# Kernel optimization log

Measured on AMD Instinct MI355X. Metric: run time of the kernel, lower is better.

## Reference

```python
import jax, jax.numpy as jnp
from jax import lax
import numpy as np
import math

# Static module config (matches init_kwargs)
K = 5            # kernel_size
MD = 3           # max_degree
HH = (MD + 1) ** 2   # n_harmonics = 16
CIN, F = 16, 32
B, D = 1, 48
NJ = K // 2      # n_radial_profiles (one shell per integer radius 1..K//2)
DN = ('NCDHW', 'OIDHW', 'NCDHW')


def _sh_table(ct, st, phi):
    """Complex spherical harmonics Y_n^m up to degree 3 (Condon-Shortley), [*grid, HH]."""
    fourpi = 4.0 * np.pi
    def N(n, m):
        return np.sqrt((2 * n + 1) / fourpi * math.factorial(n - m) / math.factorial(n + m))
    P = {
        (0, 0): np.ones_like(ct),
        (1, 0): ct,
        (1, 1): -st,
        (2, 0): 0.5 * (3 * ct ** 2 - 1),
        (2, 1): -3.0 * ct * st,
        (2, 2): 3.0 * st ** 2,
        (3, 0): 0.5 * (5 * ct ** 3 - 3 * ct),
        (3, 1): -1.5 * (5 * ct ** 2 - 1) * st,
        (3, 2): 15.0 * ct * st ** 2,
        (3, 3): -15.0 * st ** 3,
    }
    sh = np.zeros(ct.shape + (HH,), dtype=np.complex64)
    for n in range(MD + 1):
        for m in range(0, n + 1):
            y = (N(n, m) * P[(n, m)]).astype(np.complex64) * np.exp(1j * m * phi).astype(np.complex64)
            sh[..., n * n + n + m] = y
            if m > 0:
                sh[..., n * n + n - m] = ((-1) ** m) * np.conj(y)
    return sh


def _make_atoms():
    """Radial-shell x SH atoms: [K,K,K,NJ,HH] complex, L2-normalized per atom."""
    g = np.linspace(-(K // 2), K // 2, K)
    x, y, z = np.meshgrid(g, g, g, indexing='xy')
    r = np.sqrt(x * x + y * y + z * z)
    phi = np.arctan2(y, x)
    ct = np.divide(z, r, out=np.zeros_like(r), where=r != 0)
    st = np.sqrt(np.clip(1.0 - ct * ct, 0.0, None))
    sh = _sh_table(ct, st, phi)                                     # [K,K,K,HH]
    prof = np.stack([np.clip(1.0 - np.abs(r - j), 0.0, None) for j in range(1, NJ + 1)], -1)  # [K,K,K,NJ]
    atoms = prof[..., :, None] * sh[..., None, :]                   # [K,K,K,NJ,HH]
    norm = np.sqrt((np.abs(atoms) ** 2).sum(axis=(0, 1, 2), keepdims=True))
    atoms = atoms / np.where(norm > 0, norm, 1.0)
    return atoms.real.astype(np.float32), atoms.imag.astype(np.float32)


ATOMS_R, ATOMS_I = _make_atoms()
DEG = np.repeat(np.arange(MD + 1), 2 * np.arange(MD + 1) + 1)       # harmonic index -> degree (len HH)


def setup_inputs() -> dict:
    key = jax.random.key(0)
    ks = jax.random.split(key, 4)
    lim = float(np.sqrt(6.0 / (CIN + F)))
    return {
        'x': jax.random.normal(ks[0], (B, CIN, D, D, D), jnp.float32),
        'w': jax.random.uniform(ks[1], (CIN, F, NJ, MD + 1), jnp.float32, -lim, lim),
        'central_w': jax.random.uniform(ks[2], (F, CIN, 1, 1, 1), jnp.float32, -lim, lim),
        'central_b': jnp.zeros((F,), jnp.float32),
        'spec_bias': jnp.zeros(((MD + 1) * F,), jnp.float32),
        'proj_w': jax.random.uniform(ks[3], (F, (MD + 1) * F, 1, 1, 1), jnp.float32, -0.1, 0.1),
        'proj_b': jnp.zeros((F,), jnp.float32),
    }


def _forward(x, w, central_w, central_b, spec_bias, proj_w, proj_b):
    # Expand per-degree weights to per-harmonic (repeat_interleave over 2n+1 orders),
    # then fuse the per-channel SH conv + channel/radial weighted sum into a single
    # dense conv with composed kernels (same math as the torch loop + sum over axes 4,6).
    wh = w[..., DEG]                                                 # [C,F,NJ,HH]
    kr = jnp.einsum('cfjh,xyzjh->fhcxyz', wh, jnp.asarray(ATOMS_R)).reshape(F * HH, CIN, K, K, K)
    ki = jnp.einsum('cfjh,xyzjh->fhcxyz', wh, jnp.asarray(ATOMS_I)).reshape(F * HH, CIN, K, K, K)
    yr = lax.conv_general_dilated(x, kr, (1, 1, 1), 'SAME', dimension_numbers=DN)
    yi = lax.conv_general_dilated(x, ki, (1, 1, 1), 'SAME', dimension_numbers=DN)
    b, _, d, h, wd = yr.shape
    yr = yr.reshape(b, F, HH, d, h, wd)
    yi = yi.reshape(b, F, HH, d, h, wd)
    # 1x1x1 central-pixel conv added to the degree-0 (harmonic 0) real map
    cp = lax.conv_general_dilated(x, central_w, (1, 1, 1), 'SAME', dimension_numbers=DN)
    cp = cp + central_b[None, :, None, None, None]
    yr = yr.at[:, :, 0].add(cp)
    # rotation-invariant power spectrum per degree: 1/(2n+1) * sum_m (re^2 + im^2)
    p = yr * yr + yi * yi                                            # [B,F,HH,d,h,w]
    spec = jnp.stack([p[:, :, n * n:n * n + 2 * n + 1].sum(2) / (2 * n + 1) for n in range(MD + 1)], 2)
    spec = spec.reshape(b, F * (MD + 1), d, h, wd) + spec_bias[None, :, None, None, None]
    # activation=('Linear',...) is identity; projection 1x1x1 conv + ReLU
    out = lax.conv_general_dilated(spec, proj_w, (1, 1, 1), 'SAME', dimension_numbers=DN)
    out = out + proj_b[None, :, None, None, None]
    return jax.nn.relu(out)


def reference(x, w, central_w, central_b, spec_bias, proj_w, proj_b):
    return _forward(x, w, central_w, central_b, spec_bias, proj_w, proj_b)
```

## Files before the change

kernel.cpp:

```cpp
#include <hip/hip_runtime.h>
#include <hip/hip_fp16.h>
#include <math.h>


#define TX 8
#define TY 4
#define TZ 4
#define LXX 12
#define LYY 8
#define LZZ 8
#define NPOS 768
#define CPAD 24
#define POSB 48

#define ATAB2_B 0
#define WT2_B   23552
#define CW2_B   31744
#define PWT_B   32768
#define OB_B    49152
#define ED_B    49280

typedef __half2 h2;
union I4H { int4 v; h2 h[4]; };

__global__ __launch_bounds__(256) void ssh_init(
    const float* __restrict__ w, const float* __restrict__ cw,
    const float* __restrict__ proj_w, const float* __restrict__ spec_bias,
    const float* __restrict__ proj_b, char* __restrict__ wsb)
{
    __shared__ float shr[125][16];
    __shared__ float shi[125][16];
    __shared__ float prof[125][2];
    __shared__ float norms[2][16];
    __shared__ int epos[92];
    const int tid = threadIdx.x;
    const float fourpi = 4.0f * 3.14159265358979323846f;

    for (int p = tid; p < 125; p += 256) {
        int d2 = p % 5, d1 = (p / 5) % 5, d0 = p / 25;
        float xc = (float)(d1 - 2), yc = (float)(d0 - 2), zc = (float)(d2 - 2);
        float r2 = xc*xc + yc*yc + zc*zc;
        float r  = sqrtf(r2);
        float phi = atan2f(yc, xc);
        float ct = (r > 0.f) ? (zc / r) : 0.f;
        float st = sqrtf(fmaxf(0.f, 1.f - ct*ct));
        float c1 = cosf(phi), s1 = sinf(phi);
        float c2 = c1*c1 - s1*s1, s2 = 2.f*s1*c1;
        float c3 = c2*c1 - s2*s1, s3 = s2*c1 + c2*s1;
        float P10 = ct,              P11 = -st;
        float P20 = 0.5f*(3.f*ct*ct - 1.f), P21 = -3.f*ct*st, P22 = 3.f*st*st;
        float P30 = 0.5f*(5.f*ct*ct*ct - 3.f*ct);
        float P31 = -1.5f*(5.f*ct*ct - 1.f)*st;
        float P32 = 15.f*ct*st*st;
        float P33 = -15.f*st*st*st;
        float N00 = sqrtf(1.f/fourpi);
        float N10 = sqrtf(3.f/fourpi);
        float N11 = sqrtf(3.f/fourpi * 0.5f);
        float N20 = sqrtf(5.f/fourpi);
        float N21 = sqrtf(5.f/fourpi / 6.f);
        float N22 = sqrtf(5.f/fourpi / 24.f);
        float N30 = sqrtf(7.f/fourpi);
        float N31 = sqrtf(7.f/fourpi / 12.f);
        float N32 = sqrtf(7.f/fourpi / 120.f);
        float N33 = sqrtf(7.f/fourpi / 720.f);
        float b;
        shr[p][0] = N00;               shi[p][0] = 0.f;
        shr[p][2] = N10*P10;           shi[p][2] = 0.f;
        b = N11*P11;
        shr[p][3] =  b*c1;             shi[p][3] =  b*s1;
        shr[p][1] = -b*c1;             shi[p][1] =  b*s1;
        shr[p][6] = N20*P20;           shi[p][6] = 0.f;
        b = N21*P21;
        shr[p][7] =  b*c1;             shi[p][7] =  b*s1;
        shr[p][5] = -b*c1;             shi[p][5] =  b*s1;
        b = N22*P22;
        shr[p][8] =  b*c2;             shi[p][8] =  b*s2;
        shr[p][4] =  b*c2;             shi[p][4] = -b*s2;
        shr[p][12] = N30*P30;          shi[p][12] = 0.f;
        b = N31*P31;
        shr[p][13] =  b*c1;            shi[p][13] =  b*s1;
        shr[p][11] = -b*c1;            shi[p][11] =  b*s1;
        b = N32*P32;
        shr[p][14] =  b*c2;            shi[p][14] =  b*s2;
        shr[p][10] =  b*c2;            shi[p][10] = -b*s2;
        b = N33*P33;
        shr[p][15] =  b*c3;            shi[p][15] =  b*s3;
        shr[p][9]  = -b*c3;            shi[p][9]  =  b*s3;
        prof[p][0] = fmaxf(0.f, 1.f - fabsf(r - 1.f));
        prof[p][1] = fmaxf(0.f, 1.f - fabsf(r - 2.f));
    }
    __syncthreads();

    if (tid < 32) {
        int j = tid >> 4, h = tid & 15;
        float acc = 0.f;
        for (int p = 0; p < 125; ++p) {
            float pr = prof[p][j];
            acc += pr*pr*(shr[p][h]*shr[p][h] + shi[p][h]*shi[p][h]);
        }
        float nn = sqrtf(acc);
        norms[j][h] = (nn > 0.f) ? nn : 1.f;
    }
    if (tid < 125) {
        int p = tid;
        int d2 = p % 5, d1 = (p / 5) % 5, d0 = p / 25;
        int ix = d1 - 2, iy = d0 - 2, iz = d2 - 2;
        int r2i = ix*ix + iy*iy + iz*iz;
        int cls = (r2i == 1) ? 0 : (r2i == 2 || r2i == 3) ? 1
                : (r2i == 4 || r2i == 5 || r2i == 6 || r2i == 8) ? 2 : -1;
        if (cls >= 0) {
            int rank = (cls == 0) ? 0 : (cls == 1) ? 6 : 26;
            for (int q = 0; q < p; ++q) {
                int e2 = q % 5, e1 = (q / 5) % 5, e0 = q / 25;
                int jx = e1 - 2, jy = e0 - 2, jz = e2 - 2;
                int s2i = jx*jx + jy*jy + jz*jz;
                int c2i = (s2i == 1) ? 0 : (s2i == 2 || s2i == 3) ? 1
                       : (s2i == 4 || s2i == 5 || s2i == 6 || s2i == 8) ? 2 : -1;
                rank += (c2i == cls) ? 1 : 0;
            }
            epos[rank] = p;
            ((int*)(wsb + ED_B))[rank] = (d0*(LYY*LXX) + d1*LXX + d2) * POSB;
        }
    }
    __syncthreads();

    h2* at2 = (h2*)(wsb + ATAB2_B);
    for (int t = tid; t < 92*16; t += 256) {
        int e = t >> 4, h = t & 15;
        int p = epos[e];
        float c0 = prof[p][0] / norms[0][h];
        float c1v = prof[p][1] / norms[1][h];
        at2[(h*92+e)*4 + 0] = __float2half2_rn(c0*shr[p][h]);
        at2[(h*92+e)*4 + 1] = __float2half2_rn(c0*shi[p][h]);
        at2[(h*92+e)*4 + 2] = __float2half2_rn(c1v*shr[p][h]);
        at2[(h*92+e)*4 + 3] = __float2half2_rn(c1v*shi[p][h]);
    }
    h2* wt2h = (h2*)(wsb + WT2_B);
    for (int t = tid; t < 2048; t += 256) {
        int n = t >> 9, f = (t >> 4) & 31, j = (t >> 3) & 1, cp = t & 7;
        float a = w[((2*cp*32 + f)*2 + j)*4 + n];
        float b = w[(((2*cp+1)*32 + f)*2 + j)*4 + n];
        wt2h[t] = __halves2half2(__float2half(a), __float2half(b));
    }
    h2* cw2h = (h2*)(wsb + CW2_B);
    for (int t = tid; t < 256; t += 256) {
        int f = t >> 3, cp = t & 7;
        cw2h[t] = __halves2half2(__float2half(cw[f*16 + 2*cp]),
                                 __float2half(cw[f*16 + 2*cp + 1]));
    }
    float* pwT = (float*)(wsb + PWT_B);
    for (int t = tid; t < 4096; t += 256) {
        int i = t >> 5, fo = t & 31;
        pwT[t] = proj_w[fo*128 + i];
    }
    if (tid < 32) {
        float acc = proj_b[tid];
        for (int i = 0; i < 128; ++i) acc += proj_w[tid*128 + i] * spec_bias[i];
        ((float*)(wsb + OB_B))[tid] = acc;
    }
}


__device__ __forceinline__ void conv2c(const __half* __restrict__ ldsh, int baseb,
    const int4* __restrict__ aA, const int4* __restrict__ aB,
    const int* __restrict__ ed, h2 (&zA)[4][8], h2 (&zB)[4][8])
{
#pragma unroll
    for (int r = 0; r < 4; ++r)
#pragma unroll
        for (int q = 0; q < 8; ++q) { zA[r][q] = __float2half2_rn(0.f); zB[r][q] = __float2half2_rn(0.f); }

#pragma unroll 3
    for (int e = 0; e < 6; ++e) {
        I4H ca, cb_, x0, x1;
        ca.v = aA[e]; cb_.v = aB[e];
        const int4* p = (const int4*)((const char*)ldsh + baseb + ed[e]);
        x0.v = p[0]; x1.v = p[1];
#pragma unroll
        for (int q = 0; q < 4; ++q) {
            zA[0][q]   = __hfma2(ca.h[0],  x0.h[q], zA[0][q]);
            zA[1][q]   = __hfma2(ca.h[1],  x0.h[q], zA[1][q]);
            zB[0][q]   = __hfma2(cb_.h[0], x0.h[q], zB[0][q]);
            zB[1][q]   = __hfma2(cb_.h[1], x0.h[q], zB[1][q]);
            zA[0][q+4] = __hfma2(ca.h[0],  x1.h[q], zA[0][q+4]);
            zA[1][q+4] = __hfma2(ca.h[1],  x1.h[q], zA[1][q+4]);
            zB[0][q+4] = __hfma2(cb_.h[0], x1.h[q], zB[0][q+4]);
            zB[1][q+4] = __hfma2(cb_.h[1], x1.h[q], zB[1][q+4]);
        }
    }
#pragma unroll 4
    for (int e = 6; e < 26; ++e) {
        I4H ca, cb_, x0, x1;
        ca.v = aA[e]; cb_.v = aB[e];
        const int4* p = (const int4*)((const char*)ldsh + baseb + ed[e]);
        x0.v = p[0]; x1.v = p[1];
#pragma unroll
        for (int q = 0; q < 4; ++q) {
            zA[0][q]   = __hfma2(ca.h[0],  x0.h[q], zA[0][q]);
            zA[1][q]   = __hfma2(ca.h[1],  x0.h[q], zA[1][q]);
            zA[2][q]   = __hfma2(ca.h[2],  x0.h[q], zA[2][q]);
            zA[3][q]   = __hfma2(ca.h[3],  x0.h[q], zA[3][q]);
            zB[0][q]   = __hfma2(cb_.h[0], x0.h[q], zB[0][q]);
            zB[1][q]   = __hfma2(cb_.h[1], x0.h[q], zB[1][q]);
            zB[2][q]   = __hfma2(cb_.h[2], x0.h[q], zB[2][q]);
            zB[3][q]   = __hfma2(cb_.h[3], x0.h[q], zB[3][q]);
            zA[0][q+4] = __hfma2(ca.h[0],  x1.h[q], zA[0][q+4]);
            zA[1][q+4] = __hfma2(ca.h[1],  x1.h[q], zA[1][q+4]);
            zA[2][q+4] = __hfma2(ca.h[2],  x1.h[q], zA[2][q+4]);
            zA[3][q+4] = __hfma2(ca.h[3],  x1.h[q], zA[3][q+4]);
            zB[0][q+4] = __hfma2(cb_.h[0], x1.h[q], zB[0][q+4]);
            zB[1][q+4] = __hfma2(cb_.h[1], x1.h[q], zB[1][q+4]);
            zB[2][q+4] = __hfma2(cb_.h[2], x1.h[q], zB[2][q+4]);
            zB[3][q+4] = __hfma2(cb_.h[3], x1.h[q], zB[3][q+4]);
        }
    }
#pragma unroll 3
    for (int e = 26; e < 92; ++e) {
        I4H ca, cb_, x0, x1;
        ca.v = aA[e]; cb_.v = aB[e];
        const int4* p = (const int4*)((const char*)ldsh + baseb + ed[e]);
        x0.v = p[0]; x1.v = p[1];
#pragma unroll
        for (int q = 0; q < 4; ++q) {
            zA[2][q]   = __hfma2(ca.h[2],  x0.h[q], zA[2][q]);
            zA[3][q]   = __hfma2(ca.h[3],  x0.h[q], zA[3][q]);
            zB[2][q]   = __hfma2(cb_.h[2], x0.h[q], zB[2][q]);
            zB[3][q]   = __hfma2(cb_.h[3], x0.h[q], zB[3][q]);
            zA[2][q+4] = __hfma2(ca.h[2],  x1.h[q], zA[2][q+4]);
            zA[3][q+4] = __hfma2(ca.h[3],  x1.h[q], zA[3][q+4]);
            zB[2][q+4] = __hfma2(cb_.h[2], x1.h[q], zB[2][q+4]);
            zB[3][q+4] = __hfma2(cb_.h[3], x1.h[q], zB[3][q+4]);
        }
    }
}

__device__ __forceinline__ void conv1c(const __half* __restrict__ ldsh, int baseb,
    const int4* __restrict__ aA, const int* __restrict__ ed, h2 (&zA)[4][8])
{
#pragma unroll
    for (int r = 0; r < 4; ++r)
#pragma unroll
        for (int q = 0; q < 8; ++q) zA[r][q] = __float2half2_rn(0.f);

#pragma unroll 3
    for (int e = 0; e < 6; ++e) {
        I4H ca, x0, x1;
        ca.v = aA[e];
        const int4* p = (const int4*)((const char*)ldsh + baseb + ed[e]);
        x0.v = p[0]; x1.v = p[1];
#pragma unroll
        for (int q = 0; q < 4; ++q) {
            zA[0][q]   = __hfma2(ca.h[0], x0.h[q], zA[0][q]);
            zA[1][q]   = __hfma2(ca.h[1], x0.h[q], zA[1][q]);
            zA[0][q+4] = __hfma2(ca.h[0], x1.h[q], zA[0][q+4]);
            zA[1][q+4] = __hfma2(ca.h[1], x1.h[q], zA[1][q+4]);
        }
    }
#pragma unroll 4
    for (int e = 6; e < 26; ++e) {
        I4H ca, x0, x1;
        ca.v = aA[e];
        const int4* p = (const int4*)((const char*)ldsh + baseb + ed[e]);
        x0.v = p[0]; x1.v = p[1];
#pragma unroll
        for (int q = 0; q < 4; ++q) {
            zA[0][q]   = __hfma2(ca.h[0], x0.h[q], zA[0][q]);
            zA[1][q]   = __hfma2(ca.h[1], x0.h[q], zA[1][q]);
            zA[2][q]   = __hfma2(ca.h[2], x0.h[q], zA[2][q]);
            zA[3][q]   = __hfma2(ca.h[3], x0.h[q], zA[3][q]);
            zA[0][q+4] = __hfma2(ca.h[0], x1.h[q], zA[0][q+4]);
            zA[1][q+4] = __hfma2(ca.h[1], x1.h[q], zA[1][q+4]);
            zA[2][q+4] = __hfma2(ca.h[2], x1.h[q], zA[2][q+4]);
            zA[3][q+4] = __hfma2(ca.h[3], x1.h[q], zA[3][q+4]);
        }
    }
#pragma unroll 3
    for (int e = 26; e < 92; ++e) {
        I4H ca, x0, x1;
        ca.v = aA[e];
        const int4* p = (const int4*)((const char*)ldsh + baseb + ed[e]);
        x0.v = p[0]; x1.v = p[1];
#pragma unroll
        for (int q = 0; q < 4; ++q) {
            zA[2][q]   = __hfma2(ca.h[2], x0.h[q], zA[2][q]);
            zA[3][q]   = __hfma2(ca.h[3], x0.h[q], zA[3][q]);
            zA[2][q+4] = __hfma2(ca.h[2], x1.h[q], zA[2][q+4]);
            zA[3][q+4] = __hfma2(ca.h[3], x1.h[q], zA[3][q+4]);
        }
    }
}

__device__ __forceinline__ void conv2r(const __half* __restrict__ ldsh, int baseb,
    const int4* __restrict__ aA, const int4* __restrict__ aB,
    const int* __restrict__ ed, h2 (&z)[4][8])
{
#pragma unroll
    for (int r = 0; r < 4; ++r)
#pragma unroll
        for (int q = 0; q < 8; ++q) z[r][q] = __float2half2_rn(0.f);

#pragma unroll 3
    for (int e = 0; e < 6; ++e) {
        I4H ca, cb_, x0, x1;
        ca.v = aA[e]; cb_.v = aB[e];
        const int4* p = (const int4*)((const char*)ldsh + baseb + ed[e]);
        x0.v = p[0]; x1.v = p[1];
#pragma unroll
        for (int q = 0; q < 4; ++q) {
            z[0][q]   = __hfma2(ca.h[0],  x0.h[q], z[0][q]);
            z[2][q]   = __hfma2(cb_.h[0], x0.h[q], z[2][q]);
            z[0][q+4] = __hfma2(ca.h[0],  x1.h[q], z[0][q+4]);
            z[2][q+4] = __hfma2(cb_.h[0], x1.h[q], z[2][q+4]);
        }
    }
#pragma unroll 4
    for (int e = 6; e < 26; ++e) {
        I4H ca, cb_, x0, x1;
        ca.v = aA[e]; cb_.v = aB[e];
        const int4* p = (const int4*)((const char*)ldsh + baseb + ed[e]);
        x0.v = p[0]; x1.v = p[1];
#pragma unroll
        for (int q = 0; q < 4; ++q) {
            z[0][q]   = __hfma2(ca.h[0],  x0.h[q], z[0][q]);
            z[1][q]   = __hfma2(ca.h[2],  x0.h[q], z[1][q]);
            z[2][q]   = __hfma2(cb_.h[0], x0.h[q], z[2][q]);
            z[3][q]   = __hfma2(cb_.h[2], x0.h[q], z[3][q]);
            z[0][q+4] = __hfma2(ca.h[0],  x1.h[q], z[0][q+4]);
            z[1][q+4] = __hfma2(ca.h[2],  x1.h[q], z[1][q+4]);
            z[2][q+4] = __hfma2(cb_.h[0], x1.h[q], z[2][q+4]);
            z[3][q+4] = __hfma2(cb_.h[2], x1.h[q], z[3][q+4]);
        }
    }
#pragma unroll 3
    for (int e = 26; e < 92; ++e) {
        I4H ca, cb_, x0, x1;
        ca.v = aA[e]; cb_.v = aB[e];
        const int4* p = (const int4*)((const char*)ldsh + baseb + ed[e]);
        x0.v = p[0]; x1.v = p[1];
#pragma unroll
        for (int q = 0; q < 4; ++q) {
            z[1][q]   = __hfma2(ca.h[2],  x0.h[q], z[1][q]);
            z[3][q]   = __hfma2(cb_.h[2], x0.h[q], z[3][q]);
            z[1][q+4] = __hfma2(ca.h[2],  x1.h[q], z[1][q+4]);
            z[3][q+4] = __hfma2(cb_.h[2], x1.h[q], z[3][q+4]);
        }
    }
}


#define CDEL (2*(LYY*LXX) + 2*LXX + 2)

template<int N>
__device__ __forceinline__ void mixc2(const h2 (&zA)[4][8], const h2 (&zB)[4][8],
    const int4* __restrict__ wt2n, const float* __restrict__ pwT, float2 (&outa)[16])
{
    const float W = 2.f / (float)(2*N + 1);
#pragma unroll 2
    for (int f = 0; f < 32; ++f) {
        I4H w00, w01, w10, w11;
        w00.v = wt2n[f*4+0]; w01.v = wt2n[f*4+1];
        w10.v = wt2n[f*4+2]; w11.v = wt2n[f*4+3];
        h2 yrA = __float2half2_rn(0.f), yiA = __float2half2_rn(0.f);
        h2 yrB = __float2half2_rn(0.f), yiB = __float2half2_rn(0.f);
#pragma unroll
        for (int q = 0; q < 4; ++q) {
            yrA = __hfma2(w00.h[q], zA[0][q],   yrA);
            yrA = __hfma2(w01.h[q], zA[0][q+4], yrA);
            yrA = __hfma2(w10.h[q], zA[2][q],   yrA);
            yrA = __hfma2(w11.h[q], zA[2][q+4], yrA);
            yiA = __hfma2(w00.h[q], zA[1][q],   yiA);
            yiA = __hfma2(w01.h[q], zA[1][q+4], yiA);
            yiA = __hfma2(w10.h[q], zA[3][q],   yiA);
            yiA = __hfma2(w11.h[q], zA[3][q+4], yiA);
            yrB = __hfma2(w00.h[q], zB[0][q],   yrB);
            yrB = __hfma2(w01.h[q], zB[0][q+4], yrB);
            yrB = __hfma2(w10.h[q], zB[2][q],   yrB);
            yrB = __hfma2(w11.h[q], zB[2][q+4], yrB);
            yiB = __hfma2(w00.h[q], zB[1][q],   yiB);
            yiB = __hfma2(w01.h[q], zB[1][q+4], yiB);
            yiB = __hfma2(w10.h[q], zB[3][q],   yiB);
            yiB = __hfma2(w11.h[q], zB[3][q+4], yiB);
        }
        float ra = __low2float(yrA) + __high2float(yrA);
        float ia = __low2float(yiA) + __high2float(yiA);
        float rb = __low2float(yrB) + __high2float(yrB);
        float ib = __low2float(yiB) + __high2float(yiB);
        float s = (ra*ra + ia*ia + rb*rb + ib*ib) * W;
        const float2* pw2 = (const float2*)(pwT + (f*4 + N)*32);
#pragma unroll
        for (int k = 0; k < 16; ++k) {
            float2 t = pw2[k];
            outa[k].x = fmaf(t.x, s, outa[k].x);
            outa[k].y = fmaf(t.y, s, outa[k].y);
        }
    }
}

template<int RR, int N>
__device__ __forceinline__ void mix_cr(const h2 (&zC)[4][8], const h2 (&zR)[4][8],
    const int4* __restrict__ wt2n, const float* __restrict__ pwT, float2 (&outa)[16])
{
    const float Wc = 2.f / (float)(2*N + 1);
    const float Wr = 1.f / (float)(2*N + 1);
#pragma unroll 2
    for (int f = 0; f < 32; ++f) {
        I4H w00, w01, w10, w11;
        w00.v = wt2n[f*4+0]; w01.v = wt2n[f*4+1];
        w10.v = wt2n[f*4+2]; w11.v = wt2n[f*4+3];
        h2 yr = __float2half2_rn(0.f), yi = __float2half2_rn(0.f);
        h2 yR = __float2half2_rn(0.f);
#pragma unroll
        for (int q = 0; q < 4; ++q) {
            yr = __hfma2(w00.h[q], zC[0][q],   yr);
            yr = __hfma2(w01.h[q], zC[0][q+4], yr);
            yr = __hfma2(w10.h[q], zC[2][q],   yr);
            yr = __hfma2(w11.h[q], zC[2][q+4], yr);
            yi = __hfma2(w00.h[q], zC[1][q],   yi);
            yi = __hfma2(w01.h[q], zC[1][q+4], yi);
            yi = __hfma2(w10.h[q], zC[3][q],   yi);
            yi = __hfma2(w11.h[q], zC[3][q+4], yi);
            yR = __hfma2(w00.h[q], zR[RR][q],     yR);
            yR = __hfma2(w01.h[q], zR[RR][q+4],   yR);
            yR = __hfma2(w10.h[q], zR[RR+1][q],   yR);
            yR = __hfma2(w11.h[q], zR[RR+1][q+4], yR);
        }
        float rc = __low2float(yr) + __high2float(yr);
        float ic = __low2float(yi) + __high2float(yi);
        float rr = __low2float(yR) + __high2float(yR);
        float s = (rc*rc + ic*ic) * Wc + rr*rr * Wr;
        const float2* pw2 = (const float2*)(pwT + (f*4 + N)*32);
#pragma unroll
        for (int k = 0; k < 16; ++k) {
            float2 t = pw2[k];
            outa[k].x = fmaf(t.x, s, outa[k].x);
            outa[k].y = fmaf(t.y, s, outa[k].y);
        }
    }
}

template<int R, int N, bool CENTRAL>
__device__ __forceinline__ void mixr(const h2 (&z)[4][8],
    const int4* __restrict__ wt2n, const int4* __restrict__ cw2,
    const float* __restrict__ cbp, const __half* __restrict__ ldsh, int baseb,
    const float* __restrict__ pwT, float2 (&outa)[16])
{
    const float W = 1.f / (float)(2*N + 1);
    h2 xc[8];
    if (CENTRAL) {
        const int4* pc = (const int4*)((const char*)ldsh + baseb + CDEL*POSB);
        I4H xc0, xc1; xc0.v = pc[0]; xc1.v = pc[1];
#pragma unroll
        for (int q = 0; q < 4; ++q) { xc[q] = xc0.h[q]; xc[q+4] = xc1.h[q]; }
    }
#pragma unroll 2
    for (int f = 0; f < 32; ++f) {
        I4H w00, w01, w10, w11;
        w00.v = wt2n[f*4+0]; w01.v = wt2n[f*4+1];
        w10.v = wt2n[f*4+2]; w11.v = wt2n[f*4+3];
        h2 yr = __float2half2_rn(0.f);
#pragma unroll
        for (int q = 0; q < 4; ++q) {
            yr = __hfma2(w00.h[q], z[R][q],     yr);
            yr = __hfma2(w01.h[q], z[R][q+4],   yr);
            yr = __hfma2(w10.h[q], z[R+1][q],   yr);
            yr = __hfma2(w11.h[q], z[R+1][q+4], yr);
        }
        float yrf = __low2float(yr) + __high2float(yr);
        if (CENTRAL) {
            I4H c0, c1; c0.v = cw2[f*2]; c1.v = cw2[f*2+1];
            h2 acc = __float2half2_rn(0.f);
#pragma unroll
            for (int q = 0; q < 4; ++q) {
                acc = __hfma2(c0.h[q], xc[q],   acc);
                acc = __hfma2(c1.h[q], xc[q+4], acc);
            }
            yrf += cbp[f] + __low2float(acc) + __high2float(acc);
        }
        float s = yrf*yrf * W;
        const float2* pw2 = (const float2*)(pwT + (f*4 + N)*32);
#pragma unroll
        for (int k = 0; k < 16; ++k) {
            float2 t = pw2[k];
            outa[k].x = fmaf(t.x, s, outa[k].x);
            outa[k].y = fmaf(t.y, s, outa[k].y);
        }
    }
}

__global__ __launch_bounds__(512) void ssh_main(
    const float* __restrict__ x, const float* __restrict__ cb,
    const char* __restrict__ wsb, float* __restrict__ out)
{
    __shared__ __align__(16) __half ldsh[NPOS * CPAD];
    const int tid = threadIdx.x;
    const int x0 = blockIdx.x * TX, y0 = blockIdx.y * TY, z0 = blockIdx.z * TZ;

    for (int i = tid; i < NPOS * 8; i += 512) {
        int cp = i / NPOS;
        int pos = i - cp * NPOS;
        int lx = pos % LXX; int t1 = pos / LXX;
        int ly = t1 % LYY;  int lz = t1 / LYY;
        int gx = x0 + lx - 2, gy = y0 + ly - 2, gz = z0 + lz - 2;
        h2 hv = __float2half2_rn(0.f);
        if ((unsigned)gx < 48u && (unsigned)gy < 48u && (unsigned)gz < 48u) {
            int gi = ((2*cp*48 + gz)*48 + gy)*48 + gx;
            hv = __floats2half2_rn(x[gi], x[gi + 48*48*48]);
        }
        *(h2*)(ldsh + pos*CPAD + 2*cp) = hv;
    }
    __syncthreads();

    const int hg  = __builtin_amdgcn_readfirstlane(tid >> 7);
    const int vid = tid & 127;
    const int tx = vid & 7, ty = (vid >> 3) & 3, tz = vid >> 5;
    const int baseb = (tz*(LYY*LXX) + ty*LXX + tx) * POSB;

    const int4* __restrict__ atab = (const int4*)(wsb + ATAB2_B);
    const int*  __restrict__ ed   = (const int*)(wsb + ED_B);
    const int4* __restrict__ wt2  = (const int4*)(wsb + WT2_B);
    const int4* __restrict__ cw2  = (const int4*)(wsb + CW2_B);
    const float* __restrict__ pwT = (const float*)(wsb + PWT_B);
    const float* __restrict__ obase = (const float*)(wsb + OB_B);

    float2 outa[16];
#pragma unroll
    for (int k = 0; k < 16; ++k) outa[k] = make_float2(0.f, 0.f);

    h2 zA[4][8], zB[4][8];
    if (hg == 0) {
        conv2c(ldsh, baseb, atab + 13*92, atab + 14*92, ed, zA, zB);
        mixc2<3>(zA, zB, wt2 + 3*128, pwT, outa);
    } else if (hg == 1) {
        conv1c(ldsh, baseb, atab + 15*92, ed, zA);
        conv2r(ldsh, baseb, atab + 12*92, atab + 0*92, ed, zB);
        mix_cr<0,3>(zA, zB, wt2 + 3*128, pwT, outa);
        mixr<2,0,true>(zB, wt2 + 0*128, cw2, cb, ldsh, baseb, pwT, outa);
    } else if (hg == 2) {
        conv2c(ldsh, baseb, atab + 7*92, atab + 8*92, ed, zA, zB);
        mixc2<2>(zA, zB, wt2 + 2*128, pwT, outa);
    } else {
        conv2r(ldsh, baseb, atab + 6*92, atab + 2*92, ed, zA);
        conv1c(ldsh, baseb, atab + 3*92, ed, zB);
        mix_cr<2,1>(zB, zA, wt2 + 1*128, pwT, outa);
        mixr<0,2,false>(zA, wt2 + 2*128, cw2, cb, ldsh, baseb, pwT, outa);
    }

    __syncthreads();
    float* lmerge = (float*)ldsh;
    if (hg == 1) {
#pragma unroll
        for (int k = 0; k < 16; ++k) {
            lmerge[vid*33 + 2*k]     = outa[k].x;
            lmerge[vid*33 + 2*k + 1] = outa[k].y;
        }
    } else if (hg == 3) {
#pragma unroll
        for (int k = 0; k < 16; ++k) {
            lmerge[4224 + vid*33 + 2*k]     = outa[k].x;
            lmerge[4224 + vid*33 + 2*k + 1] = outa[k].y;
        }
    }
    __syncthreads();
    if (hg == 0) {
#pragma unroll
        for (int k = 0; k < 16; ++k) {
            outa[k].x += lmerge[vid*33 + 2*k];
            outa[k].y += lmerge[vid*33 + 2*k + 1];
        }
    } else if (hg == 2) {
#pragma unroll
        for (int k = 0; k < 16; ++k) {
            outa[k].x += lmerge[4224 + vid*33 + 2*k];
            outa[k].y += lmerge[4224 + vid*33 + 2*k + 1];
        }
#pragma unroll
        for (int k = 0; k < 16; ++k) {
            lmerge[4224 + vid*33 + 2*k]     = outa[k].x;
            lmerge[4224 + vid*33 + 2*k + 1] = outa[k].y;
        }
    }
    __syncthreads();
    if (hg == 0) {
        const int gz = z0 + tz, gy = y0 + ty, gx = x0 + tx;
#pragma unroll
        for (int k = 0; k < 16; ++k) {
            float v0 = obase[2*k]   + outa[k].x + lmerge[4224 + vid*33 + 2*k];
            float v1 = obase[2*k+1] + outa[k].y + lmerge[4224 + vid*33 + 2*k + 1];
            out[(((2*k)*48   + gz)*48 + gy)*48 + gx] = fmaxf(v0, 0.f);
            out[(((2*k+1)*48 + gz)*48 + gy)*48 + gx] = fmaxf(v1, 0.f);
        }
    }
}

extern "C" void kernel_launch(void* const* d_in, const int* in_sizes, int n_in,
                              void* d_out, int out_size, void* d_ws, size_t ws_size,
                              hipStream_t stream) {
    const float* x  = (const float*)d_in[0];
    const float* w  = (const float*)d_in[1];
    const float* cw = (const float*)d_in[2];
    const float* cb = (const float*)d_in[3];
    const float* sb = (const float*)d_in[4];
    const float* pw = (const float*)d_in[5];
    const float* pb = (const float*)d_in[6];
    float* out = (float*)d_out;
    char* wsb = (char*)d_ws;

    ssh_init<<<dim3(1), dim3(256), 0, stream>>>(w, cw, pw, sb, pb, wsb);
    ssh_main<<<dim3(48/TX, 48/TY, 48/TZ), dim3(512), 0, stream>>>(x, cb, wsb, out);
}
```

Measured before the change: 159.5 us.

## Exploit point-reflection parity of SH atoms to halve convolution taps

Spherical harmonics of odd degree are odd under point reflection and even degrees are even, so each tap pair (p, -p) is folded by adding or subtracting the two input samples before multiplying by one coefficient. The atom table shrinks from 92 to 46 entries per harmonic, and the convolution routines are regrouped by parity, with odd-degree harmonics sharing a subtract-folded pass and even ones an add-folded pass. This roughly halves the half2 FMA count and the coefficient loads, while keeping the same number of LDS input reads plus one extra add per element. Summing two fp16 samples first may slightly change rounding.

Result: slower. 199.5 us (+25.0%).

```diff
diff --git a/kernel.cpp b/kernel.cpp
--- a/kernel.cpp
+++ b/kernel.cpp
@@ -13,7 +13,7 @@
 #define CPAD 24
 #define POSB 48
 
-#define ATAB2_B 0
+#define PAT_B   0
 #define WT2_B   23552
 #define CW2_B   31744
 #define PWT_B   32768
@@ -32,7 +32,7 @@
     __shared__ float shi[125][16];
     __shared__ float prof[125][2];
     __shared__ float norms[2][16];
-    __shared__ int epos[92];
+    __shared__ int pepos[46];
     const int tid = threadIdx.x;
     const float fourpi = 4.0f * 3.14159265358979323846f;
 
@@ -101,7 +101,7 @@
         float nn = sqrtf(acc);
         norms[j][h] = (nn > 0.f) ? nn : 1.f;
     }
-    if (tid < 125) {
+    if (tid < 62) {
         int p = tid;
         int d2 = p % 5, d1 = (p / 5) % 5, d0 = p / 25;
         int ix = d1 - 2, iy = d0 - 2, iz = d2 - 2;
@@ -109,7 +109,7 @@
         int cls = (r2i == 1) ? 0 : (r2i == 2 || r2i == 3) ? 1
                 : (r2i == 4 || r2i == 5 || r2i == 6 || r2i == 8) ? 2 : -1;
         if (cls >= 0) {
-            int rank = (cls == 0) ? 0 : (cls == 1) ? 6 : 26;
+            int rank = (cls == 0) ? 0 : (cls == 1) ? 3 : 13;
             for (int q = 0; q < p; ++q) {
                 int e2 = q % 5, e1 = (q / 5) % 5, e0 = q / 25;
                 int jx = e1 - 2, jy = e0 - 2, jz = e2 - 2;
@@ -118,22 +118,23 @@
                        : (s2i == 4 || s2i == 5 || s2i == 6 || s2i == 8) ? 2 : -1;
                 rank += (c2i == cls) ? 1 : 0;
             }
-            epos[rank] = p;
-            ((int*)(wsb + ED_B))[rank] = (d0*(LYY*LXX) + d1*LXX + d2) * POSB;
+            pepos[rank] = p;
+            ((int*)(wsb + ED_B))[rank]      = (d0*(LYY*LXX) + d1*LXX + d2) * POSB;
+            ((int*)(wsb + ED_B))[46 + rank] = ((4-d0)*(LYY*LXX) + (4-d1)*LXX + (4-d2)) * POSB;
         }
     }
     __syncthreads();
 
-    h2* at2 = (h2*)(wsb + ATAB2_B);
-    for (int t = tid; t < 92*16; t += 256) {
-        int e = t >> 4, h = t & 15;
-        int p = epos[e];
+    h2* pat = (h2*)(wsb + PAT_B);
+    for (int t = tid; t < 46*16; t += 256) {
+        int h = t / 46, k = t - h*46;
+        int p = pepos[k];
         float c0 = prof[p][0] / norms[0][h];
         float c1v = prof[p][1] / norms[1][h];
-        at2[(h*92+e)*4 + 0] = __float2half2_rn(c0*shr[p][h]);
-        at2[(h*92+e)*4 + 1] = __float2half2_rn(c0*shi[p][h]);
-        at2[(h*92+e)*4 + 2] = __float2half2_rn(c1v*shr[p][h]);
-        at2[(h*92+e)*4 + 3] = __float2half2_rn(c1v*shi[p][h]);
+        pat[(h*46+k)*4 + 0] = __float2half2_rn(c0*shr[p][h]);
+        pat[(h*46+k)*4 + 1] = __float2half2_rn(c0*shi[p][h]);
+        pat[(h*46+k)*4 + 2] = __float2half2_rn(c1v*shr[p][h]);
+        pat[(h*46+k)*4 + 3] = __float2half2_rn(c1v*shi[p][h]);
     }
     h2* wt2h = (h2*)(wsb + WT2_B);
     for (int t = tid; t < 2048; t += 256) {
@@ -160,189 +161,190 @@
     }
 }
 
-
-__device__ __forceinline__ void conv2c(const __half* __restrict__ ldsh, int baseb,
+template<bool SUB>
+__device__ __forceinline__ void mkps(const __half* __restrict__ ldsh, int baseb,
+                                     int dp, int dm, h2 (&s)[8])
+{
+    const int4* pp = (const int4*)((const char*)ldsh + baseb + dp);
+    const int4* pm = (const int4*)((const char*)ldsh + baseb + dm);
+    I4H xp0, xp1, xm0, xm1;
+    xp0.v = pp[0]; xp1.v = pp[1]; xm0.v = pm[0]; xm1.v = pm[1];
+#pragma unroll
+    for (int q = 0; q < 4; ++q) {
+        s[q]   = SUB ? __hsub2(xp0.h[q], xm0.h[q]) : __hadd2(xp0.h[q], xm0.h[q]);
+        s[q+4] = SUB ? __hsub2(xp1.h[q], xm1.h[q]) : __hadd2(xp1.h[q], xm1.h[q]);
+    }
+}
+
+
+template<bool SUB>
+__device__ __forceinline__ void conv2c_p(const __half* __restrict__ ldsh, int baseb,
     const int4* __restrict__ aA, const int4* __restrict__ aB,
-    const int* __restrict__ ed, h2 (&zA)[4][8], h2 (&zB)[4][8])
+    const int* __restrict__ edp, const int* __restrict__ edm,
+    h2 (&zA)[4][8], h2 (&zB)[4][8])
 {
 #pragma unroll
     for (int r = 0; r < 4; ++r)
 #pragma unroll
         for (int q = 0; q < 8; ++q) { zA[r][q] = __float2half2_rn(0.f); zB[r][q] = __float2half2_rn(0.f); }
 
-#pragma unroll 3
-    for (int e = 0; e < 6; ++e) {
-        I4H ca, cb_, x0, x1;
-        ca.v = aA[e]; cb_.v = aB[e];
-        const int4* p = (const int4*)((const char*)ldsh + baseb + ed[e]);
-        x0.v = p[0]; x1.v = p[1];
-#pragma unroll
-        for (int q = 0; q < 4; ++q) {
-            zA[0][q]   = __hfma2(ca.h[0],  x0.h[q], zA[0][q]);
-            zA[1][q]   = __hfma2(ca.h[1],  x0.h[q], zA[1][q]);
-            zB[0][q]   = __hfma2(cb_.h[0], x0.h[q], zB[0][q]);
-            zB[1][q]   = __hfma2(cb_.h[1], x0.h[q], zB[1][q]);
-            zA[0][q+4] = __hfma2(ca.h[0],  x1.h[q], zA[0][q+4]);
-            zA[1][q+4] = __hfma2(ca.h[1],  x1.h[q], zA[1][q+4]);
-            zB[0][q+4] = __hfma2(cb_.h[0], x1.h[q], zB[0][q+4]);
-            zB[1][q+4] = __hfma2(cb_.h[1], x1.h[q], zB[1][q+4]);
-        }
-    }
-#pragma unroll 4
-    for (int e = 6; e < 26; ++e) {
-        I4H ca, cb_, x0, x1;
-        ca.v = aA[e]; cb_.v = aB[e];
-        const int4* p = (const int4*)((const char*)ldsh + baseb + ed[e]);
-        x0.v = p[0]; x1.v = p[1];
-#pragma unroll
-        for (int q = 0; q < 4; ++q) {
-            zA[0][q]   = __hfma2(ca.h[0],  x0.h[q], zA[0][q]);
-            zA[1][q]   = __hfma2(ca.h[1],  x0.h[q], zA[1][q]);
-            zA[2][q]   = __hfma2(ca.h[2],  x0.h[q], zA[2][q]);
-            zA[3][q]   = __hfma2(ca.h[3],  x0.h[q], zA[3][q]);
-            zB[0][q]   = __hfma2(cb_.h[0], x0.h[q], zB[0][q]);
-            zB[1][q]   = __hfma2(cb_.h[1], x0.h[q], zB[1][q]);
-            zB[2][q]   = __hfma2(cb_.h[2], x0.h[q], zB[2][q]);
-            zB[3][q]   = __hfma2(cb_.h[3], x0.h[q], zB[3][q]);
-            zA[0][q+4] = __hfma2(ca.h[0],  x1.h[q], zA[0][q+4]);
-            zA[1][q+4] = __hfma2(ca.h[1],  x1.h[q], zA[1][q+4]);
-            zA[2][q+4] = __hfma2(ca.h[2],  x1.h[q], zA[2][q+4]);
-            zA[3][q+4] = __hfma2(ca.h[3],  x1.h[q], zA[3][q+4]);
-            zB[0][q+4] = __hfma2(cb_.h[0], x1.h[q], zB[0][q+4]);
-            zB[1][q+4] = __hfma2(cb_.h[1], x1.h[q], zB[1][q+4]);
-            zB[2][q+4] = __hfma2(cb_.h[2], x1.h[q], zB[2][q+4]);
-            zB[3][q+4] = __hfma2(cb_.h[3], x1.h[q], zB[3][q+4]);
-        }
-    }
-#pragma unroll 3
-    for (int e = 26; e < 92; ++e) {
-        I4H ca, cb_, x0, x1;
-        ca.v = aA[e]; cb_.v = aB[e];
-        const int4* p = (const int4*)((const char*)ldsh + baseb + ed[e]);
-        x0.v = p[0]; x1.v = p[1];
-#pragma unroll
-        for (int q = 0; q < 4; ++q) {
-            zA[2][q]   = __hfma2(ca.h[2],  x0.h[q], zA[2][q]);
-            zA[3][q]   = __hfma2(ca.h[3],  x0.h[q], zA[3][q]);
-            zB[2][q]   = __hfma2(cb_.h[2], x0.h[q], zB[2][q]);
-            zB[3][q]   = __hfma2(cb_.h[3], x0.h[q], zB[3][q]);
-            zA[2][q+4] = __hfma2(ca.h[2],  x1.h[q], zA[2][q+4]);
-            zA[3][q+4] = __hfma2(ca.h[3],  x1.h[q], zA[3][q+4]);
-            zB[2][q+4] = __hfma2(cb_.h[2], x1.h[q], zB[2][q+4]);
-            zB[3][q+4] = __hfma2(cb_.h[3], x1.h[q], zB[3][q+4]);
-        }
-    }
-}
-
-__device__ __forceinline__ void conv1c(const __half* __restrict__ ldsh, int baseb,
-    const int4* __restrict__ aA, const int* __restrict__ ed, h2 (&zA)[4][8])
-{
-#pragma unroll
-    for (int r = 0; r < 4; ++r)
-#pragma unroll
-        for (int q = 0; q < 8; ++q) zA[r][q] = __float2half2_rn(0.f);
-
-#pragma unroll 3
-    for (int e = 0; e < 6; ++e) {
-        I4H ca, x0, x1;
-        ca.v = aA[e];
-        const int4* p = (const int4*)((const char*)ldsh + baseb + ed[e]);
-        x0.v = p[0]; x1.v = p[1];
-#pragma unroll
-        for (int q = 0; q < 4; ++q) {
-            zA[0][q]   = __hfma2(ca.h[0], x0.h[q], zA[0][q]);
-            zA[1][q]   = __hfma2(ca.h[1], x0.h[q], zA[1][q]);
-            zA[0][q+4] = __hfma2(ca.h[0], x1.h[q], zA[0][q+4]);
-            zA[1][q+4] = __hfma2(ca.h[1], x1.h[q], zA[1][q+4]);
-        }
-    }
-#pragma unroll 4
-    for (int e = 6; e < 26; ++e) {
-        I4H ca, x0, x1;
-        ca.v = aA[e];
-        const int4* p = (const int4*)((const char*)ldsh + baseb + ed[e]);
-        x0.v = p[0]; x1.v = p[1];
-#pragma unroll
-        for (int q = 0; q < 4; ++q) {
-            zA[0][q]   = __hfma2(ca.h[0], x0.h[q], zA[0][q]);
-            zA[1][q]   = __hfma2(ca.h[1], x0.h[q], zA[1][q]);
-            zA[2][q]   = __hfma2(ca.h[2], x0.h[q], zA[2][q]);
-            zA[3][q]   = __hfma2(ca.h[3], x0.h[q], zA[3][q]);
-            zA[0][q+4] = __hfma2(ca.h[0], x1.h[q], zA[0][q+4]);
-            zA[1][q+4] = __hfma2(ca.h[1], x1.h[q], zA[1][q+4]);
-            zA[2][q+4] = __hfma2(ca.h[2], x1.h[q], zA[2][q+4]);
-            zA[3][q+4] = __hfma2(ca.h[3], x1.h[q], zA[3][q+4]);
-        }
-    }
-#pragma unroll 3
-    for (int e = 26; e < 92; ++e) {
-        I4H ca, x0, x1;
-        ca.v = aA[e];
-        const int4* p = (const int4*)((const char*)ldsh + baseb + ed[e]);
-        x0.v = p[0]; x1.v = p[1];
-#pragma unroll
-        for (int q = 0; q < 4; ++q) {
-            zA[2][q]   = __hfma2(ca.h[2], x0.h[q], zA[2][q]);
-            zA[3][q]   = __hfma2(ca.h[3], x0.h[q], zA[3][q]);
-            zA[2][q+4] = __hfma2(ca.h[2], x1.h[q], zA[2][q+4]);
-            zA[3][q+4] = __hfma2(ca.h[3], x1.h[q], zA[3][q+4]);
-        }
-    }
-}
-
-__device__ __forceinline__ void conv2r(const __half* __restrict__ ldsh, int baseb,
-    const int4* __restrict__ aA, const int4* __restrict__ aB,
-    const int* __restrict__ ed, h2 (&z)[4][8])
-{
-#pragma unroll
-    for (int r = 0; r < 4; ++r)
-#pragma unroll
-        for (int q = 0; q < 8; ++q) z[r][q] = __float2half2_rn(0.f);
-
-#pragma unroll 3
-    for (int e = 0; e < 6; ++e) {
-        I4H ca, cb_, x0, x1;
-        ca.v = aA[e]; cb_.v = aB[e];
-        const int4* p = (const int4*)((const char*)ldsh + baseb + ed[e]);
-        x0.v = p[0]; x1.v = p[1];
-#pragma unroll
-        for (int q = 0; q < 4; ++q) {
-            z[0][q]   = __hfma2(ca.h[0],  x0.h[q], z[0][q]);
-            z[2][q]   = __hfma2(cb_.h[0], x0.h[q], z[2][q]);
-            z[0][q+4] = __hfma2(ca.h[0],  x1.h[q], z[0][q+4]);
-            z[2][q+4] = __hfma2(cb_.h[0], x1.h[q], z[2][q+4]);
-        }
-    }
-#pragma unroll 4
-    for (int e = 6; e < 26; ++e) {
-        I4H ca, cb_, x0, x1;
-        ca.v = aA[e]; cb_.v = aB[e];
-        const int4* p = (const int4*)((const char*)ldsh + baseb + ed[e]);
-        x0.v = p[0]; x1.v = p[1];
-#pragma unroll
-        for (int q = 0; q < 4; ++q) {
-            z[0][q]   = __hfma2(ca.h[0],  x0.h[q], z[0][q]);
-            z[1][q]   = __hfma2(ca.h[2],  x0.h[q], z[1][q]);
-            z[2][q]   = __hfma2(cb_.h[0], x0.h[q], z[2][q]);
-            z[3][q]   = __hfma2(cb_.h[2], x0.h[q], z[3][q]);
-            z[0][q+4] = __hfma2(ca.h[0],  x1.h[q], z[0][q+4]);
-            z[1][q+4] = __hfma2(ca.h[2],  x1.h[q], z[1][q+4]);
-            z[2][q+4] = __hfma2(cb_.h[0], x1.h[q], z[2][q+4]);
-            z[3][q+4] = __hfma2(cb_.h[2], x1.h[q], z[3][q+4]);
-        }
-    }
-#pragma unroll 3
-    for (int e = 26; e < 92; ++e) {
-        I4H ca, cb_, x0, x1;
-        ca.v = aA[e]; cb_.v = aB[e];
-        const int4* p = (const int4*)((const char*)ldsh + baseb + ed[e]);
-        x0.v = p[0]; x1.v = p[1];
-#pragma unroll
-        for (int q = 0; q < 4; ++q) {
-            z[1][q]   = __hfma2(ca.h[2],  x0.h[q], z[1][q]);
-            z[3][q]   = __hfma2(cb_.h[2], x0.h[q], z[3][q]);
-            z[1][q+4] = __hfma2(ca.h[2],  x1.h[q], z[1][q+4]);
-            z[3][q+4] = __hfma2(cb_.h[2], x1.h[q], z[3][q+4]);
+#pragma unroll
+    for (int k = 0; k < 3; ++k) {
+        I4H ca, cb_; ca.v = aA[k]; cb_.v = aB[k];
+        h2 s[8]; mkps<SUB>(ldsh, baseb, edp[k], edm[k], s);
+#pragma unroll
+        for (int q = 0; q < 4; ++q) {
+            zA[0][q]   = __hfma2(ca.h[0],  s[q],   zA[0][q]);
+            zA[1][q]   = __hfma2(ca.h[1],  s[q],   zA[1][q]);
+            zB[0][q]   = __hfma2(cb_.h[0], s[q],   zB[0][q]);
+            zB[1][q]   = __hfma2(cb_.h[1], s[q],   zB[1][q]);
+            zA[0][q+4] = __hfma2(ca.h[0],  s[q+4], zA[0][q+4]);
+            zA[1][q+4] = __hfma2(ca.h[1],  s[q+4], zA[1][q+4]);
+            zB[0][q+4] = __hfma2(cb_.h[0], s[q+4], zB[0][q+4]);
+            zB[1][q+4] = __hfma2(cb_.h[1], s[q+4], zB[1][q+4]);
+        }
+    }
+#pragma unroll 2
+    for (int k = 3; k < 13; ++k) {
+        I4H ca, cb_; ca.v = aA[k]; cb_.v = aB[k];
+        h2 s[8]; mkps<SUB>(ldsh, baseb, edp[k], edm[k], s);
+#pragma unroll
+        for (int q = 0; q < 4; ++q) {
+            zA[0][q]   = __hfma2(ca.h[0],  s[q],   zA[0][q]);
+            zA[1][q]   = __hfma2(ca.h[1],  s[q],   zA[1][q]);
+            zA[2][q]   = __hfma2(ca.h[2],  s[q],   zA[2][q]);
+            zA[3][q]   = __hfma2(ca.h[3],  s[q],   zA[3][q]);
+            zB[0][q]   = __hfma2(cb_.h[0], s[q],   zB[0][q]);
+            zB[1][q]   = __hfma2(cb_.h[1], s[q],   zB[1][q]);
+            zB[2][q]   = __hfma2(cb_.h[2], s[q],   zB[2][q]);
+            zB[3][q]   = __hfma2(cb_.h[3], s[q],   zB[3][q]);
+            zA[0][q+4] = __hfma2(ca.h[0],  s[q+4], zA[0][q+4]);
+            zA[1][q+4] = __hfma2(ca.h[1],  s[q+4], zA[1][q+4]);
+            zA[2][q+4] = __hfma2(ca.h[2],  s[q+4], zA[2][q+4]);
+            zA[3][q+4] = __hfma2(ca.h[3],  s[q+4], zA[3][q+4]);
+            zB[0][q+4] = __hfma2(cb_.h[0], s[q+4], zB[0][q+4]);
+            zB[1][q+4] = __hfma2(cb_.h[1], s[q+4], zB[1][q+4]);
+            zB[2][q+4] = __hfma2(cb_.h[2], s[q+4], zB[2][q+4]);
+            zB[3][q+4] = __hfma2(cb_.h[3], s[q+4], zB[3][q+4]);
+        }
+    }
+#pragma unroll 2
+    for (int k = 13; k < 46; ++k) {
+        I4H ca, cb_; ca.v = aA[k]; cb_.v = aB[k];
+        h2 s[8]; mkps<SUB>(ldsh, baseb, edp[k], edm[k], s);
+#pragma unroll
+        for (int q = 0; q < 4; ++q) {
+            zA[2][q]   = __hfma2(ca.h[2],  s[q],   zA[2][q]);
+            zA[3][q]   = __hfma2(ca.h[3],  s[q],   zA[3][q]);
+            zB[2][q]   = __hfma2(cb_.h[2], s[q],   zB[2][q]);
+            zB[3][q]   = __hfma2(cb_.h[3], s[q],   zB[3][q]);
+            zA[2][q+4] = __hfma2(ca.h[2],  s[q+4], zA[2][q+4]);
+            zA[3][q+4] = __hfma2(ca.h[3],  s[q+4], zA[3][q+4]);
+            zB[2][q+4] = __hfma2(cb_.h[2], s[q+4], zB[2][q+4]);
+            zB[3][q+4] = __hfma2(cb_.h[3], s[q+4], zB[3][q+4]);
+        }
+    }
+}
+
+template<bool SUB>
+__device__ __forceinline__ void conv_cr_p(const __half* __restrict__ ldsh, int baseb,
+    const int4* __restrict__ aC, const int4* __restrict__ aR,
+    const int* __restrict__ edp, const int* __restrict__ edm,
+    h2 (&zC)[4][8], h2 (&zR)[2][8])
+{
+#pragma unroll
+    for (int q = 0; q < 8; ++q) {
+        zC[0][q] = __float2half2_rn(0.f); zC[1][q] = __float2half2_rn(0.f);
+        zC[2][q] = __float2half2_rn(0.f); zC[3][q] = __float2half2_rn(0.f);
+        zR[0][q] = __float2half2_rn(0.f); zR[1][q] = __float2half2_rn(0.f);
+    }
+#pragma unroll
+    for (int k = 0; k < 3; ++k) {
+        I4H cc, cr; cc.v = aC[k]; cr.v = aR[k];
+        h2 s[8]; mkps<SUB>(ldsh, baseb, edp[k], edm[k], s);
+#pragma unroll
+        for (int q = 0; q < 4; ++q) {
+            zC[0][q]   = __hfma2(cc.h[0], s[q],   zC[0][q]);
+            zC[1][q]   = __hfma2(cc.h[1], s[q],   zC[1][q]);
+            zR[0][q]   = __hfma2(cr.h[0], s[q],   zR[0][q]);
+            zC[0][q+4] = __hfma2(cc.h[0], s[q+4], zC[0][q+4]);
+            zC[1][q+4] = __hfma2(cc.h[1], s[q+4], zC[1][q+4]);
+            zR[0][q+4] = __hfma2(cr.h[0], s[q+4], zR[0][q+4]);
+        }
+    }
+#pragma unroll 2
+    for (int k = 3; k < 13; ++k) {
+        I4H cc, cr; cc.v = aC[k]; cr.v = aR[k];
+        h2 s[8]; mkps<SUB>(ldsh, baseb, edp[k], edm[k], s);
+#pragma unroll
+        for (int q = 0; q < 4; ++q) {
+            zC[0][q]   = __hfma2(cc.h[0], s[q],   zC[0][q]);
+            zC[1][q]   = __hfma2(cc.h[1], s[q],   zC[1][q]);
+            zC[2][q]   = __hfma2(cc.h[2], s[q],   zC[2][q]);
+            zC[3][q]   = __hfma2(cc.h[3], s[q],   zC[3][q]);
+            zR[0][q]   = __hfma2(cr.h[0], s[q],   zR[0][q]);
+            zR[1][q]   = __hfma2(cr.h[2], s[q],   zR[1][q]);
+            zC[0][q+4] = __hfma2(cc.h[0], s[q+4], zC[0][q+4]);
+            zC[1][q+4] = __hfma2(cc.h[1], s[q+4], zC[1][q+4]);
+            zC[2][q+4] = __hfma2(cc.h[2], s[q+4], zC[2][q+4]);
+            zC[3][q+4] = __hfma2(cc.h[3], s[q+4], zC[3][q+4]);
+            zR[0][q+4] = __hfma2(cr.h[0], s[q+4], zR[0][q+4]);
+            zR[1][q+4] = __hfma2(cr.h[2], s[q+4], zR[1][q+4]);
+        }
+    }
+#pragma unroll 2
+    for (int k = 13; k < 46; ++k) {
+        I4H cc, cr; cc.v = aC[k]; cr.v = aR[k];
+        h2 s[8]; mkps<SUB>(ldsh, baseb, edp[k], edm[k], s);
+#pragma unroll
+        for (int q = 0; q < 4; ++q) {
+            zC[2][q]   = __hfma2(cc.h[2], s[q],   zC[2][q]);
+            zC[3][q]   = __hfma2(cc.h[3], s[q],   zC[3][q]);
+            zR[1][q]   = __hfma2(cr.h[2], s[q],   zR[1][q]);
+            zC[2][q+4] = __hfma2(cc.h[2], s[q+4], zC[2][q+4]);
+            zC[3][q+4] = __hfma2(cc.h[3], s[q+4], zC[3][q+4]);
+            zR[1][q+4] = __hfma2(cr.h[2], s[q+4], zR[1][q+4]);
+        }
+    }
+}
+
+template<bool SUB>
+__device__ __forceinline__ void conv1r_p(const __half* __restrict__ ldsh, int baseb,
+    const int4* __restrict__ aR,
+    const int* __restrict__ edp, const int* __restrict__ edm, h2 (&zR)[2][8])
+{
+#pragma unroll
+    for (int q = 0; q < 8; ++q) { zR[0][q] = __float2half2_rn(0.f); zR[1][q] = __float2half2_rn(0.f); }
+#pragma unroll
+    for (int k = 0; k < 3; ++k) {
+        I4H cr; cr.v = aR[k];
+        h2 s[8]; mkps<SUB>(ldsh, baseb, edp[k], edm[k], s);
+#pragma unroll
+        for (int q = 0; q < 4; ++q) {
+            zR[0][q]   = __hfma2(cr.h[0], s[q],   zR[0][q]);
+            zR[0][q+4] = __hfma2(cr.h[0], s[q+4], zR[0][q+4]);
+        }
+    }
+#pragma unroll 2
+    for (int k = 3; k < 13; ++k) {
+        I4H cr; cr.v = aR[k];
+        h2 s[8]; mkps<SUB>(ldsh, baseb, edp[k], edm[k], s);
+#pragma unroll
+        for (int q = 0; q < 4; ++q) {
+            zR[0][q]   = __hfma2(cr.h[0], s[q],   zR[0][q]);
+            zR[1][q]   = __hfma2(cr.h[2], s[q],   zR[1][q]);
+            zR[0][q+4] = __hfma2(cr.h[0], s[q+4], zR[0][q+4]);
+            zR[1][q+4] = __hfma2(cr.h[2], s[q+4], zR[1][q+4]);
+        }
+    }
+#pragma unroll 2
+    for (int k = 13; k < 46; ++k) {
+        I4H cr; cr.v = aR[k];
+        h2 s[8]; mkps<SUB>(ldsh, baseb, edp[k], edm[k], s);
+#pragma unroll
+        for (int q = 0; q < 4; ++q) {
+            zR[1][q]   = __hfma2(cr.h[2], s[q],   zR[1][q]);
+            zR[1][q+4] = __hfma2(cr.h[2], s[q+4], zR[1][q+4]);
         }
     }
 }
@@ -396,8 +398,8 @@
     }
 }
 
-template<int RR, int N>
-__device__ __forceinline__ void mix_cr(const h2 (&zC)[4][8], const h2 (&zR)[4][8],
+template<int N>
+__device__ __forceinline__ void mix_cr(const h2 (&zC)[4][8], const h2 (&zR)[2][8],
     const int4* __restrict__ wt2n, const float* __restrict__ pwT, float2 (&outa)[16])
 {
     const float Wc = 2.f / (float)(2*N + 1);
@@ -419,10 +421,10 @@
             yi = __hfma2(w01.h[q], zC[1][q+4], yi);
             yi = __hfma2(w10.h[q], zC[3][q],   yi);
             yi = __hfma2(w11.h[q], zC[3][q+4], yi);
-            yR = __hfma2(w00.h[q], zR[RR][q],     yR);
-            yR = __hfma2(w01.h[q], zR[RR][q+4],   yR);
-            yR = __hfma2(w10.h[q], zR[RR+1][q],   yR);
-            yR = __hfma2(w11.h[q], zR[RR+1][q+4], yR);
+            yR = __hfma2(w00.h[q], zR[0][q],   yR);
+            yR = __hfma2(w01.h[q], zR[0][q+4], yR);
+            yR = __hfma2(w10.h[q], zR[1][q],   yR);
+            yR = __hfma2(w11.h[q], zR[1][q+4], yR);
         }
         float rc = __low2float(yr) + __high2float(yr);
         float ic = __low2float(yi) + __high2float(yi);
@@ -438,8 +440,8 @@
     }
 }
 
-template<int R, int N, bool CENTRAL>
-__device__ __forceinline__ void mixr(const h2 (&z)[4][8],
+template<int N, bool CENTRAL>
+__device__ __forceinline__ void mixr(const h2 (&z)[2][8],
     const int4* __restrict__ wt2n, const int4* __restrict__ cw2,
     const float* __restrict__ cbp, const __half* __restrict__ ldsh, int baseb,
     const float* __restrict__ pwT, float2 (&outa)[16])
@@ -460,10 +462,10 @@
         h2 yr = __float2half2_rn(0.f);
 #pragma unroll
         for (int q = 0; q < 4; ++q) {
-            yr = __hfma2(w00.h[q], z[R][q],     yr);
-            yr = __hfma2(w01.h[q], z[R][q+4],   yr);
-            yr = __hfma2(w10.h[q], z[R+1][q],   yr);
-            yr = __hfma2(w11.h[q], z[R+1][q+4], yr);
+            yr = __hfma2(w00.h[q], z[0][q],   yr);
+            yr = __hfma2(w01.h[q], z[0][q+4], yr);
+            yr = __hfma2(w10.h[q], z[1][q],   yr);
+            yr = __hfma2(w11.h[q], z[1][q+4], yr);
         }
         float yrf = __low2float(yr) + __high2float(yr);
         if (CENTRAL) {
@@ -515,8 +517,9 @@
     const int tx = vid & 7, ty = (vid >> 3) & 3, tz = vid >> 5;
     const int baseb = (tz*(LYY*LXX) + ty*LXX + tx) * POSB;
 
-    const int4* __restrict__ atab = (const int4*)(wsb + ATAB2_B);
-    const int*  __restrict__ ed   = (const int*)(wsb + ED_B);
+    const int4* __restrict__ pat  = (const int4*)(wsb + PAT_B);
+    const int*  __restrict__ edp  = (const int*)(wsb + ED_B);
+    const int*  __restrict__ edm  = edp + 46;
     const int4* __restrict__ wt2  = (const int4*)(wsb + WT2_B);
     const int4* __restrict__ cw2  = (const int4*)(wsb + CW2_B);
     const float* __restrict__ pwT = (const float*)(wsb + PWT_B);
@@ -526,23 +529,28 @@
 #pragma unroll
     for (int k = 0; k < 16; ++k) outa[k] = make_float2(0.f, 0.f);
 
-    h2 zA[4][8], zB[4][8];
     if (hg == 0) {
-        conv2c(ldsh, baseb, atab + 13*92, atab + 14*92, ed, zA, zB);
+        h2 zA[4][8], zB[4][8];
+        conv2c_p<true>(ldsh, baseb, pat + 13*46, pat + 14*46, edp, edm, zA, zB);
         mixc2<3>(zA, zB, wt2 + 3*128, pwT, outa);
     } else if (hg == 1) {
-        conv1c(ldsh, baseb, atab + 15*92, ed, zA);
-        conv2r(ldsh, baseb, atab + 12*92, atab + 0*92, ed, zB);
-        mix_cr<0,3>(zA, zB, wt2 + 3*128, pwT, outa);
-        mixr<2,0,true>(zB, wt2 + 0*128, cw2, cb, ldsh, baseb, pwT, outa);
+        h2 zC[4][8], zR[2][8];
+        conv_cr_p<true>(ldsh, baseb, pat + 15*46, pat + 12*46, edp, edm, zC, zR);
+        mix_cr<3>(zC, zR, wt2 + 3*128, pwT, outa);
+        h2 zR0[2][8];
+        conv1r_p<false>(ldsh, baseb, pat + 0*46, edp, edm, zR0);
+        mixr<0,true>(zR0, wt2 + 0*128, cw2, cb, ldsh, baseb, pwT, outa);
     } else if (hg == 2) {
-        conv2c(ldsh, baseb, atab + 7*92, atab + 8*92, ed, zA, zB);
+        h2 zA[4][8], zB[4][8];
+        conv2c_p<false>(ldsh, baseb, pat + 7*46, pat + 8*46, edp, edm, zA, zB);
         mixc2<2>(zA, zB, wt2 + 2*128, pwT, outa);
     } else {
-        conv2r(ldsh, baseb, atab + 6*92, atab + 2*92, ed, zA);
-        conv1c(ldsh, baseb, atab + 3*92, ed, zB);
-        mix_cr<2,1>(zB, zA, wt2 + 1*128, pwT, outa);
-        mixr<0,2,false>(zA, wt2 + 2*128, cw2, cb, ldsh, baseb, pwT, outa);
+        h2 zC[4][8], zR[2][8];
+        conv_cr_p<true>(ldsh, baseb, pat + 3*46, pat + 2*46, edp, edm, zC, zR);
+        mix_cr<1>(zC, zR, wt2 + 1*128, pwT, outa);
+        h2 zR0[2][8];
+        conv1r_p<false>(ldsh, baseb, pat + 6*46, edp, edm, zR0);
+        mixr<2,false>(zR0, wt2 + 2*128, cw2, cb, ldsh, baseb, pwT, outa);
     }
 
     __syncthreads();
```
